# Kernel tuning notes

Hardware: AMD Instinct MI355X
Metric: run time of the kernel (lower is better)

## Reference

```python
import jax, jax.numpy as jnp
import numpy as np
from jax import lax


def _attend(Wq, bq, h, key_mat, value, mask):
    # key_mat: [B, A, T], value: [B, T, Vd], h: [B, H], mask: [B, T]
    q = h @ Wq.T + bq                             # [B, A]
    energy = jnp.einsum('ba,bat->bt', q, key_mat)  # [B, T]
    att = jax.nn.softmax(energy, axis=-1) * mask
    att = att / jnp.sum(att, axis=-1, keepdims=True)
    ctx = jnp.einsum('bt,btv->bv', att, value)     # [B, Vd]
    return att, ctx


def setup_inputs() -> dict:
    B, T, H, A, Vd, V, L = 32, 512, 512, 128, 512, 32000, 100
    CD = H + Vd  # concat_dim
    root = jax.random.key(0)
    ks = jax.random.split(root, 20)
    s = 0.02
    inp = {
        'key': jax.random.normal(ks[0], (B, A, T), jnp.float32),
        'value': jax.random.normal(ks[1], (B, T, Vd), jnp.float32),
        'Yinput': jax.random.randint(ks[2], (B, L), 0, V),
        'max_len': L,
        'src_lens': jax.random.randint(ks[3], (B,), 1, T + 1),
        'W_emb': jax.random.normal(ks[4], (V, H), jnp.float32) * s,
        'b_proj': jnp.zeros((V,), jnp.float32),
        'Wq': jax.random.normal(ks[5], (A, H), jnp.float32) * s,
        'bq': jnp.zeros((A,), jnp.float32),
        'W_ih': jax.random.normal(ks[6], (4 * H, CD), jnp.float32) * s,
        'W_hh': jax.random.normal(ks[7], (4 * H, H), jnp.float32) * s,
        'b_ih': jnp.zeros((4 * H,), jnp.float32),
        'b_hh': jnp.zeros((4 * H,), jnp.float32),
        'Wm': jax.random.normal(ks[8], (H, CD), jnp.float32) * s,
        'bm': jnp.zeros((H,), jnp.float32),
        'h00': jax.random.normal(ks[9], (1, H), jnp.float32) * s,
        'c00': jax.random.normal(ks[10], (1, H), jnp.float32) * s,
    }
    return inp


def reference(key, value, Yinput, max_len, src_lens, W_emb, b_proj, Wq, bq,
              W_ih, W_hh, b_ih, b_hh, Wm, bm, h00, c00):
    B, A, T = key.shape
    H = h00.shape[1]
    mask = (jnp.arange(T)[None, :] < src_lens[:, None]).astype(key.dtype)  # [B, T]

    h = jnp.broadcast_to(h00, (B, H))
    c = jnp.broadcast_to(c00, (B, H))
    _, ctx = _attend(Wq, bq, h, key, value, mask)
    idx = jnp.zeros((B,), jnp.int32)  # greedy decode, start token 0 (eval mode)

    def step(carry, _):
        h, c, ctx, idx = carry
        emb = W_emb[idx]                                   # [B, H]
        x = jnp.concatenate([emb, ctx], axis=-1)           # [B, H+Vd]
        # torch.nn.LSTMCell gate math (i, f, g, o order)
        gates = x @ W_ih.T + b_ih + h @ W_hh.T + b_hh      # [B, 4H]
        i, f, g, o = jnp.split(gates, 4, axis=-1)
        c1 = jax.nn.sigmoid(f) * c + jax.nn.sigmoid(i) * jnp.tanh(g)
        h1 = jax.nn.sigmoid(o) * jnp.tanh(c1)
        _, ctx1 = _attend(Wq, bq, h1, key, value, mask)
        cat2 = jnp.concatenate([c1, ctx1], axis=-1)        # note: uses c1 (as in source)
        proj = jax.nn.leaky_relu(cat2 @ Wm.T + bm, negative_slope=0.01)
        pred = jax.nn.log_softmax(proj @ W_emb.T + b_proj, axis=-1)  # tied weights
        idx1 = jnp.argmax(pred, axis=-1).astype(jnp.int32)
        return (h1, c1, ctx1, idx1), pred

    _, preds = lax.scan(step, (h, c, ctx, idx), None, length=int(max_len))
    return jnp.transpose(preds, (1, 0, 2))  # [B, max_len, V]
```

## Files before the change

### kernel.cpp

```cpp
#include <hip/hip_runtime.h>
#include <math.h>

#define B_  32
#define T_  512
#define H_  512
#define A_  128
#define VD_ 512
#define V_  32000
#define NCHUNK 500

__device__ __forceinline__ float sigf(float x){ return 1.f/(1.f+expf(-x)); }
__device__ __forceinline__ float dot4(float4 a, float4 b){ return a.x*b.x+a.y*b.y+a.z*b.z+a.w*b.w; }

struct DecArgs {
  const float *key, *value, *W_emb, *b_proj, *Wq, *bq, *W_ih, *W_hh, *b_ih, *b_hh, *Wm, *bm, *h00, *c00;
  const int* src_lens;
  float* out;
  float *hA, *hB, *c, *ctx, *projT, *logits, *lse, *pm, *ps;
  int *pidx, *idx;
  int L;
};

__global__ void k_init(DecArgs P) {
  int g = blockIdx.x*256 + threadIdx.x;
  if (g < B_*H_) { P.hA[g] = P.h00[g & (H_-1)]; P.c[g] = P.c00[g & (H_-1)]; }
  if (g < B_) P.idx[g] = 0;
}

__global__ __launch_bounds__(256) void k_gatesout(DecArgs P, const float* hin,
                                                  float* hout, int s) {
  __shared__ float sm[3200];
  int bid = blockIdx.x, tid = threadIdx.x;
  if (bid < 256) {
    float* Wl   = sm;
    float* xl   = sm + 576;
    float* part = sm + 2880;
    int*   idx_sh = (int*)(sm + 3168);
    const int kp = tid >> 5, jr = (tid >> 2) & 7, bg = tid & 3;
    if (tid < 32) idx_sh[tid] = P.idx[tid];
    float acc[8];
#pragma unroll
    for (int i = 0; i < 8; i++) acc[i] = 0.f;

    for (int w = 0; w < 24; w++) {
      __syncthreads();
      if (tid < 128) {
        int r = tid >> 4, i = tid & 15;
        int g = r >> 1, tl = r & 1;
        int j = g*512 + bid*2 + tl;
        const float4* src = (w < 16)
          ? (const float4*)(P.W_ih + (size_t)j*1024) + w*16 + i
          : (const float4*)(P.W_hh + (size_t)j*512) + (w-16)*16 + i;
        float4 x = *src;
        int kb = i*4;
        Wl[(kb+0)*9+r]=x.x; Wl[(kb+1)*9+r]=x.y; Wl[(kb+2)*9+r]=x.z; Wl[(kb+3)*9+r]=x.w;
      }
      {
        int q = tid*2;
#pragma unroll
        for (int u = 0; u < 2; u++, q++) {
          int b = q >> 4, i = q & 15;
          float4 x;
          if (w < 8)       x = *((const float4*)(P.W_emb + (size_t)idx_sh[b]*512) + w*16 + i);
          else if (w < 16) x = *((const float4*)(P.ctx + b*512) + (w-8)*16 + i);
          else             x = *((const float4*)(hin  + b*512) + (w-16)*16 + i);
          int kb = i*4;
          xl[(kb+0)*36+b]=x.x; xl[(kb+1)*36+b]=x.y; xl[(kb+2)*36+b]=x.z; xl[(kb+3)*36+b]=x.w;
        }
      }
      __syncthreads();
#pragma unroll
      for (int kk = 0; kk < 8; kk++) {
        int kl = kp*8 + kk;
        float wv = Wl[kl*9 + jr];
        const float4* xv = (const float4*)(xl + kl*36 + bg*8);
        float4 a0 = xv[0], a1 = xv[1];
        acc[0] += wv*a0.x; acc[1] += wv*a0.y; acc[2] += wv*a0.z; acc[3] += wv*a0.w;
        acc[4] += wv*a1.x; acc[5] += wv*a1.y; acc[6] += wv*a1.z; acc[7] += wv*a1.w;
      }
    }
    __syncthreads();
    for (int rd = 0; rd < 8; rd++) {
      if (kp == rd) {
        float* pr = part + jr*36 + bg*8;
        if (rd == 0) {
#pragma unroll
          for (int u = 0; u < 8; u++) pr[u] = acc[u];
        } else {
#pragma unroll
          for (int u = 0; u < 8; u++) pr[u] += acc[u];
        }
      }
      __syncthreads();
    }
    if (tid < 64) {
      int tl = tid >> 5, b = tid & 31;
      int t = bid*2 + tl;
      float gi = part[(0+tl)*36 + b] + P.b_ih[0*512+t] + P.b_hh[0*512+t];
      float gf = part[(2+tl)*36 + b] + P.b_ih[1*512+t] + P.b_hh[1*512+t];
      float gg = part[(4+tl)*36 + b] + P.b_ih[2*512+t] + P.b_hh[2*512+t];
      float go = part[(6+tl)*36 + b] + P.b_ih[3*512+t] + P.b_hh[3*512+t];
      float c0 = P.c[b*H_ + t];
      float c1 = sigf(gf)*c0 + sigf(gi)*tanhf(gg);
      P.c[b*H_ + t] = c1;
      hout[b*H_ + t] = sigf(go)*tanhf(c1);
    }
  } else if (s > 0) {
    int r = bid - 256;
    int bb = r >> 3, vs = r & 7;
    float l = P.lse[bb];
    const float4* lg = (const float4*)(P.logits + (size_t)bb*V_ + vs*4000);
    float4* o4 = (float4*)(P.out + ((size_t)bb*P.L + (s-1))*V_ + vs*4000);
    for (int i = tid; i < 1000; i += 256) {
      float4 x = lg[i];
      o4[i] = make_float4(x.x-l, x.y-l, x.z-l, x.w-l);
    }
  }
}

__global__ __launch_bounds__(256) void k_att(DecArgs P, const float* hsrc) {
  __shared__ float sf[1408];
  int bid = blockIdx.x, tid = threadIdx.x;
  int b = bid & 31, vs = bid >> 5;
  float* h_sh   = sf;
  float* q_sh   = sf + 512;
  float* red    = sf + 640;
  float* att_sh = sf + 896;
  h_sh[tid]       = hsrc[b*H_ + tid];
  h_sh[tid + 256] = hsrc[b*H_ + tid + 256];
  __syncthreads();
  if (tid < 128) {
    const float4* hv = (const float4*)h_sh;
    const float4* w  = (const float4*)(P.Wq + (size_t)tid*H_);
    float acc = P.bq[tid];
#pragma unroll 8
    for (int k = 0; k < 128; k++) acc += dot4(w[k], hv[k]);
    q_sh[tid] = acc;
  }
  __syncthreads();
  const float* kp = P.key + (size_t)b*A_*T_;
  float e0 = 0.f, e1 = 0.f;
#pragma unroll 8
  for (int a = 0; a < A_; a++) {
    float qa = q_sh[a];
    e0 += qa * kp[a*T_ + tid];
    e1 += qa * kp[a*T_ + tid + 256];
  }
  red[tid] = fmaxf(e0, e1);
  __syncthreads();
  for (int s2 = 128; s2 > 0; s2 >>= 1) { if (tid < s2) red[tid] = fmaxf(red[tid], red[tid+s2]); __syncthreads(); }
  float M = red[0];
  __syncthreads();
  int len = P.src_lens[b];
  float p0 = (tid       < len) ? expf(e0 - M) : 0.f;
  float p1 = (tid + 256 < len) ? expf(e1 - M) : 0.f;
  red[tid] = p0 + p1;
  __syncthreads();
  for (int s2 = 128; s2 > 0; s2 >>= 1) { if (tid < s2) red[tid] += red[tid+s2]; __syncthreads(); }
  float S = red[0];
  __syncthreads();
  att_sh[tid]       = p0 / S;
  att_sh[tid + 256] = p1 / S;
  __syncthreads();
  int vl = tid & 63, tq = tid >> 6;
  int v = vs*64 + vl;
  const float* vp = P.value + (size_t)b*T_*VD_ + v;
  float acc = 0.f;
  int t0 = tq*128;
#pragma unroll 8
  for (int t = t0; t < t0 + 128; t++) acc += att_sh[t] * vp[(size_t)t*VD_];
  red[tid] = acc;
  __syncthreads();
  if (tid < 64) P.ctx[b*VD_ + vs*64 + tid] = red[tid] + red[tid+64] + red[tid+128] + red[tid+192];
}

__global__ __launch_bounds__(256) void k_proj(DecArgs P) {
  __shared__ float sm[2600];
  int bid = blockIdx.x, tid = threadIdx.x;
  float* Wl   = sm;
  float* xl   = sm + 192;
  float* part = sm + 2496;
  const int kp = tid >> 5, ml = (tid >> 4) & 1, bg = tid & 15;
  float acc0 = 0.f, acc1 = 0.f;

  for (int w = 0; w < 16; w++) {
    __syncthreads();
    if (tid < 32) {
      int r = tid >> 4, i = tid & 15;
      float4 x = *((const float4*)(P.Wm + (size_t)(bid*2+r)*1024) + w*16 + i);
      int kb = i*4;
      Wl[(kb+0)*3+r]=x.x; Wl[(kb+1)*3+r]=x.y; Wl[(kb+2)*3+r]=x.z; Wl[(kb+3)*3+r]=x.w;
    }
    {
      int q = tid*2;
#pragma unroll
      for (int u = 0; u < 2; u++, q++) {
        int b = q >> 4, i = q & 15;
        float4 x = (w < 8) ? *((const float4*)(P.c + b*512) + w*16 + i)
                           : *((const float4*)(P.ctx + b*512) + (w-8)*16 + i);
        int kb = i*4;
        xl[(kb+0)*36+b]=x.x; xl[(kb+1)*36+b]=x.y; xl[(kb+2)*36+b]=x.z; xl[(kb+3)*36+b]=x.w;
      }
    }
    __syncthreads();
#pragma unroll
    for (int kk = 0; kk < 8; kk++) {
      int kl = kp*8 + kk;
      float wv = Wl[kl*3 + ml];
      acc0 += wv * xl[kl*36 + bg*2];
      acc1 += wv * xl[kl*36 + bg*2 + 1];
    }
  }
  __syncthreads();
  for (int rd = 0; rd < 8; rd++) {
    if (kp == rd) {
      float* pr = part + ml*36 + bg*2;
      if (rd == 0) { pr[0] = acc0; pr[1] = acc1; }
      else         { pr[0] += acc0; pr[1] += acc1; }
    }
    __syncthreads();
  }
  if (tid < 64) {
    int ml2 = tid >> 5, b = tid & 31;
    int m = bid*2 + ml2;
    float s = part[ml2*36 + b] + P.bm[m];
    P.projT[m*32 + b] = (s > 0.f) ? s : 0.01f*s;
  }
}

__global__ __launch_bounds__(256) void k_logits(DecArgs P) {
  __shared__ float sm[9600];
  int bid = blockIdx.x, tid = threadIdx.x;
  const int v0 = bid * 64;
  float* Wl   = sm;
  float* pl   = sm + 4352;
  float* part = sm + 6400;
  const int kp = tid >> 5, vg = (tid >> 2) & 7, bg = tid & 3;
  const int sr = tid >> 2, skq = tid & 3;
  float acc[64];
#pragma unroll
  for (int i = 0; i < 64; i++) acc[i] = 0.f;

  const float* wrow = P.W_emb + (size_t)(v0 + sr)*H_ + skq*16;
  const float4* pbase = (const float4*)P.projT;
  float4 t0 = *((const float4*)(wrow + 0));
  float4 t1 = *((const float4*)(wrow + 4));
  float4 t2 = *((const float4*)(wrow + 8));
  float4 t3 = *((const float4*)(wrow + 12));
  float4 u0 = pbase[tid];
  float4 u1 = pbase[tid + 256];

  for (int w = 0; w < 8; w++) {
    __syncthreads();
    int kb = skq*16;
    Wl[(kb+ 0)*68+sr]=t0.x; Wl[(kb+ 1)*68+sr]=t0.y; Wl[(kb+ 2)*68+sr]=t0.z; Wl[(kb+ 3)*68+sr]=t0.w;
    Wl[(kb+ 4)*68+sr]=t1.x; Wl[(kb+ 5)*68+sr]=t1.y; Wl[(kb+ 6)*68+sr]=t1.z; Wl[(kb+ 7)*68+sr]=t1.w;
    Wl[(kb+ 8)*68+sr]=t2.x; Wl[(kb+ 9)*68+sr]=t2.y; Wl[(kb+10)*68+sr]=t2.z; Wl[(kb+11)*68+sr]=t2.w;
    Wl[(kb+12)*68+sr]=t3.x; Wl[(kb+13)*68+sr]=t3.y; Wl[(kb+14)*68+sr]=t3.z; Wl[(kb+15)*68+sr]=t3.w;
    ((float4*)pl)[tid]       = u0;
    ((float4*)pl)[tid + 256] = u1;
    __syncthreads();
    if (w < 7) {
      const float* wn = wrow + (w+1)*64;
      t0 = *((const float4*)(wn + 0));
      t1 = *((const float4*)(wn + 4));
      t2 = *((const float4*)(wn + 8));
      t3 = *((const float4*)(wn + 12));
      u0 = pbase[(w+1)*512 + tid];
      u1 = pbase[(w+1)*512 + tid + 256];
    }
#pragma unroll
    for (int kk = 0; kk < 8; kk++) {
      int kl = kp*8 + kk;
      float4 wv0 = *((const float4*)(Wl + kl*68 + vg*8));
      float4 wv1 = *((const float4*)(Wl + kl*68 + vg*8 + 4));
      float4 pv0 = *((const float4*)(pl + kl*32 + bg*8));
      float4 pv1 = *((const float4*)(pl + kl*32 + bg*8 + 4));
      float wa[8] = {wv0.x,wv0.y,wv0.z,wv0.w,wv1.x,wv1.y,wv1.z,wv1.w};
      float pa[8] = {pv0.x,pv0.y,pv0.z,pv0.w,pv1.x,pv1.y,pv1.z,pv1.w};
#pragma unroll
      for (int i = 0; i < 8; i++)
#pragma unroll
        for (int j = 0; j < 8; j++)
          acc[i*8+j] += wa[i]*pa[j];
    }
  }
  __syncthreads();
  if (kp == 0) {
#pragma unroll
    for (int j = 0; j < 8; j++) {
      int b = bg*8 + j;
      *((float4*)(part + b*68 + vg*8))     = make_float4(acc[0*8+j], acc[1*8+j], acc[2*8+j], acc[3*8+j]);
      *((float4*)(part + b*68 + vg*8 + 4)) = make_float4(acc[4*8+j], acc[5*8+j], acc[6*8+j], acc[7*8+j]);
    }
  }
  __syncthreads();
  for (int rd = 1; rd < 8; rd++) {
    if (kp == rd) {
#pragma unroll
      for (int j = 0; j < 8; j++) {
        int b = bg*8 + j;
        float4* q0 = (float4*)(part + b*68 + vg*8);
        float4* q1 = q0 + 1;
        float4 a0 = *q0, a1 = *q1;
        a0.x += acc[0*8+j]; a0.y += acc[1*8+j]; a0.z += acc[2*8+j]; a0.w += acc[3*8+j];
        a1.x += acc[4*8+j]; a1.y += acc[5*8+j]; a1.z += acc[6*8+j]; a1.w += acc[7*8+j];
        *q0 = a0; *q1 = a1;
      }
    }
    __syncthreads();
  }
  int b = tid >> 3, vq = tid & 7;
  float4 pA = *((const float4*)(part + b*68 + vq*8));
  float4 pB = *((const float4*)(part + b*68 + vq*8 + 4));
  int vb = v0 + vq*8;
  float x[8] = {pA.x,pA.y,pA.z,pA.w,pB.x,pB.y,pB.z,pB.w};
#pragma unroll
  for (int i = 0; i < 8; i++) x[i] += P.b_proj[vb + i];
  *((float4*)(P.logits + (size_t)b*V_ + vb))     = make_float4(x[0],x[1],x[2],x[3]);
  *((float4*)(P.logits + (size_t)b*V_ + vb + 4)) = make_float4(x[4],x[5],x[6],x[7]);
  float m = x[0], s = 1.f; int mi = vb;
#pragma unroll
  for (int i = 1; i < 8; i++) {
    if (x[i] > m) { s = s*expf(m - x[i]) + 1.f; m = x[i]; mi = vb + i; }
    else          { s += expf(x[i] - m); }
  }
  float* rm = sm; float* rs = sm + 256; int* ri = (int*)(sm + 512);
  __syncthreads();
  rm[vq*32 + b] = m; rs[vq*32 + b] = s; ri[vq*32 + b] = mi;
  __syncthreads();
  if (tid < 32) {
    int bb = tid;
    float M = rm[bb], S = rs[bb]; int I = ri[bb];
#pragma unroll
    for (int g = 1; g < 8; g++) {
      float m2 = rm[g*32+bb], s2 = rs[g*32+bb]; int i2 = ri[g*32+bb];
      if (m2 > M)       { S = S*expf(M - m2) + s2; M = m2; I = i2; }
      else if (m2 == M) { S += s2; I = min(I, i2); }
      else              { S += s2*expf(m2 - M); }
    }
    P.pm[bid*32 + bb] = M; P.ps[bid*32 + bb] = S; P.pidx[bid*32 + bb] = I;
  }
}

__global__ __launch_bounds__(256) void k_merge(DecArgs P) {
  __shared__ float sfm[256], sfs[256];
  __shared__ int   sii[256];
  int b = blockIdx.x, tid = threadIdx.x;
  float M = P.pm[tid*32 + b], S = P.ps[tid*32 + b]; int I = P.pidx[tid*32 + b];
  int c2 = tid + 256;
  if (c2 < NCHUNK) {
    float m2 = P.pm[c2*32+b], s2 = P.ps[c2*32+b]; int i2 = P.pidx[c2*32+b];
    if (m2 > M)       { S = S*expf(M - m2) + s2; M = m2; I = i2; }
    else if (m2 == M) { S += s2; I = min(I, i2); }
    else              { S += s2*expf(m2 - M); }
  }
  sfm[tid] = M; sfs[tid] = S; sii[tid] = I;
  __syncthreads();
  for (int st = 128; st > 0; st >>= 1) {
    if (tid < st) {
      float m1 = sfm[tid], s1 = sfs[tid]; int i1 = sii[tid];
      float m2 = sfm[tid+st], s2 = sfs[tid+st]; int i2 = sii[tid+st];
      float Mn, Sn; int In;
      if (m2 > m1)      { Mn = m2; Sn = s1*expf(m1-m2) + s2; In = i2; }
      else if (m2 < m1) { Mn = m1; Sn = s1 + s2*expf(m2-m1); In = i1; }
      else              { Mn = m1; Sn = s1 + s2; In = min(i1, i2); }
      sfm[tid] = Mn; sfs[tid] = Sn; sii[tid] = In;
    }
    __syncthreads();
  }
  if (tid == 0) { P.lse[b] = sfm[0] + logf(sfs[0]); P.idx[b] = sii[0]; }
}

__global__ __launch_bounds__(256) void k_finalout(DecArgs P) {
  int bid = blockIdx.x, tid = threadIdx.x;
  int b = bid & 31, vs = bid >> 5;
  float l = P.lse[b];
  const float4* lg = (const float4*)(P.logits + (size_t)b*V_ + vs*4000);
  float4* o4 = (float4*)(P.out + ((size_t)b*P.L + (P.L-1))*V_ + vs*4000);
  for (int i = tid; i < 1000; i += 256) {
    float4 x = lg[i];
    o4[i] = make_float4(x.x-l, x.y-l, x.z-l, x.w-l);
  }
}

extern "C" void kernel_launch(void* const* d_in, const int* in_sizes, int n_in,
                              void* d_out, int out_size, void* d_ws, size_t ws_size,
                              hipStream_t stream) {
  DecArgs P;
  P.key      = (const float*)d_in[0];
  P.value    = (const float*)d_in[1];
  P.src_lens = (const int*)d_in[4];
  P.W_emb    = (const float*)d_in[5];
  P.b_proj   = (const float*)d_in[6];
  P.Wq       = (const float*)d_in[7];
  P.bq       = (const float*)d_in[8];
  P.W_ih     = (const float*)d_in[9];
  P.W_hh     = (const float*)d_in[10];
  P.b_ih     = (const float*)d_in[11];
  P.b_hh     = (const float*)d_in[12];
  P.Wm       = (const float*)d_in[13];
  P.bm       = (const float*)d_in[14];
  P.h00      = (const float*)d_in[15];
  P.c00      = (const float*)d_in[16];
  P.out      = (float*)d_out;
  P.L        = in_sizes[2] / B_;

  float* ws = (float*)d_ws;
  P.hA     = ws; ws += B_*H_;
  P.hB     = ws; ws += B_*H_;
  P.c      = ws; ws += B_*H_;
  P.ctx    = ws; ws += B_*VD_;
  P.projT  = ws; ws += H_*B_;
  P.lse    = ws; ws += 32;
  P.pm     = ws; ws += NCHUNK*B_;
  P.ps     = ws; ws += NCHUNK*B_;
  P.logits = ws; ws += (size_t)B_*V_;
  P.pidx   = (int*)ws; ws += NCHUNK*B_;
  P.idx    = (int*)ws;

  k_init<<<64, 256, 0, stream>>>(P);
  k_att<<<256, 256, 0, stream>>>(P, P.hA);

  for (int s = 0; s < P.L; s++) {
    const float* hin  = (s & 1) ? P.hB : P.hA;
    float*       hout = (s & 1) ? P.hA : P.hB;
    k_gatesout<<<512, 256, 0, stream>>>(P, hin, hout, s);
    k_att<<<256, 256, 0, stream>>>(P, hout);
    k_proj<<<256, 256, 0, stream>>>(P);
    k_logits<<<NCHUNK, 256, 0, stream>>>(P);
    k_merge<<<32, 256, 0, stream>>>(P);
  }
  k_finalout<<<256, 256, 0, stream>>>(P);
}
```

Measured before the change: 10.08 ms.

## Prefetch gate tiles into registers, widen attention grid, fold merge into logits

```diff
diff --git a/kernel.cpp b/kernel.cpp
--- a/kernel.cpp
+++ b/kernel.cpp
@@ -18,6 +18,7 @@
   float* out;
   float *hA, *hB, *c, *ctx, *projT, *logits, *lse, *pm, *ps;
   int *pidx, *idx;
+  int* bar;
   int L;
 };
 
@@ -41,34 +42,58 @@
     float acc[8];
 #pragma unroll
     for (int i = 0; i < 8; i++) acc[i] = 0.f;
+    __syncthreads();
+
+    const int r = tid >> 4, iW = tid & 15;
+    const int gW = r >> 1, tlW = r & 1;
+    const int jW = gW*512 + bid*2 + tlW;
+    float4 wreg; float4 xreg[2];
+    {
+      if (tid < 128) wreg = *((const float4*)(P.W_ih + (size_t)jW*1024) + iW);
+      int q = tid*2;
+#pragma unroll
+      for (int u = 0; u < 2; u++) {
+        int b = (q+u) >> 4, i = (q+u) & 15;
+        xreg[u] = *((const float4*)(P.W_emb + (size_t)idx_sh[b]*512) + i);
+      }
+    }
 
     for (int w = 0; w < 24; w++) {
       __syncthreads();
       if (tid < 128) {
-        int r = tid >> 4, i = tid & 15;
-        int g = r >> 1, tl = r & 1;
-        int j = g*512 + bid*2 + tl;
-        const float4* src = (w < 16)
-          ? (const float4*)(P.W_ih + (size_t)j*1024) + w*16 + i
-          : (const float4*)(P.W_hh + (size_t)j*512) + (w-16)*16 + i;
-        float4 x = *src;
-        int kb = i*4;
-        Wl[(kb+0)*9+r]=x.x; Wl[(kb+1)*9+r]=x.y; Wl[(kb+2)*9+r]=x.z; Wl[(kb+3)*9+r]=x.w;
+        int kb = iW*4;
+        Wl[(kb+0)*9+r]=wreg.x; Wl[(kb+1)*9+r]=wreg.y; Wl[(kb+2)*9+r]=wreg.z; Wl[(kb+3)*9+r]=wreg.w;
       }
       {
         int q = tid*2;
 #pragma unroll
-        for (int u = 0; u < 2; u++, q++) {
-          int b = q >> 4, i = q & 15;
-          float4 x;
-          if (w < 8)       x = *((const float4*)(P.W_emb + (size_t)idx_sh[b]*512) + w*16 + i);
-          else if (w < 16) x = *((const float4*)(P.ctx + b*512) + (w-8)*16 + i);
-          else             x = *((const float4*)(hin  + b*512) + (w-16)*16 + i);
+        for (int u = 0; u < 2; u++) {
+          int b = (q+u) >> 4, i = (q+u) & 15;
           int kb = i*4;
-          xl[(kb+0)*36+b]=x.x; xl[(kb+1)*36+b]=x.y; xl[(kb+2)*36+b]=x.z; xl[(kb+3)*36+b]=x.w;
+          xl[(kb+0)*36+b]=xreg[u].x; xl[(kb+1)*36+b]=xreg[u].y;
+          xl[(kb+2)*36+b]=xreg[u].z; xl[(kb+3)*36+b]=xreg[u].w;
         }
       }
       __syncthreads();
+      if (w < 23) {
+        int w1 = w + 1;
+        if (tid < 128) {
+          const float4* src = (w1 < 16)
+            ? (const float4*)(P.W_ih + (size_t)jW*1024) + w1*16 + iW
+            : (const float4*)(P.W_hh + (size_t)jW*512) + (w1-16)*16 + iW;
+          wreg = *src;
+        }
+        int q = tid*2;
+#pragma unroll
+        for (int u = 0; u < 2; u++) {
+          int b = (q+u) >> 4, i = (q+u) & 15;
+          const float4* src;
+          if (w1 < 8)       src = (const float4*)(P.W_emb + (size_t)idx_sh[b]*512) + w1*16 + i;
+          else if (w1 < 16) src = (const float4*)(P.ctx + b*512) + (w1-8)*16 + i;
+          else              src = (const float4*)(hin  + b*512) + (w1-16)*16 + i;
+          xreg[u] = *src;
+        }
+      }
 #pragma unroll
       for (int kk = 0; kk < 8; kk++) {
         int kl = kp*8 + kk;
@@ -106,8 +131,8 @@
       hout[b*H_ + t] = sigf(go)*tanhf(c1);
     }
   } else if (s > 0) {
-    int r = bid - 256;
-    int bb = r >> 3, vs = r & 7;
+    int r2 = bid - 256;
+    int bb = r2 >> 3, vs = r2 & 7;
     float l = P.lse[bb];
     const float4* lg = (const float4*)(P.logits + (size_t)bb*V_ + vs*4000);
     float4* o4 = (float4*)(P.out + ((size_t)bb*P.L + (s-1))*V_ + vs*4000);
@@ -129,14 +154,17 @@
   h_sh[tid]       = hsrc[b*H_ + tid];
   h_sh[tid + 256] = hsrc[b*H_ + tid + 256];
   __syncthreads();
-  if (tid < 128) {
-    const float4* hv = (const float4*)h_sh;
-    const float4* w  = (const float4*)(P.Wq + (size_t)tid*H_);
-    float acc = P.bq[tid];
+  {
+    int a = tid & 127, half = tid >> 7;
+    const float4* hv = (const float4*)h_sh + half*64;
+    const float4* w  = (const float4*)(P.Wq + (size_t)a*H_) + half*64;
+    float acc = 0.f;
 #pragma unroll 8
-    for (int k = 0; k < 128; k++) acc += dot4(w[k], hv[k]);
-    q_sh[tid] = acc;
-  }
+    for (int k = 0; k < 64; k++) acc += dot4(w[k], hv[k]);
+    red[tid] = acc;
+  }
+  __syncthreads();
+  if (tid < 128) q_sh[tid] = red[tid] + red[128 + tid] + P.bq[tid];
   __syncthreads();
   const float* kp = P.key + (size_t)b*A_*T_;
   float e0 = 0.f, e1 = 0.f;
@@ -146,6 +174,7 @@
     e0 += qa * kp[a*T_ + tid];
     e1 += qa * kp[a*T_ + tid + 256];
   }
+  __syncthreads();
   red[tid] = fmaxf(e0, e1);
   __syncthreads();
   for (int s2 = 128; s2 > 0; s2 >>= 1) { if (tid < s2) red[tid] = fmaxf(red[tid], red[tid+s2]); __syncthreads(); }
@@ -162,16 +191,20 @@
   att_sh[tid]       = p0 / S;
   att_sh[tid + 256] = p1 / S;
   __syncthreads();
-  int vl = tid & 63, tq = tid >> 6;
-  int v = vs*64 + vl;
-  const float* vp = P.value + (size_t)b*T_*VD_ + v;
+  int vl = tid & 31, tq = tid >> 5;
+  const float* vp = P.value + (size_t)b*T_*VD_ + vs*32 + vl;
   float acc = 0.f;
-  int t0 = tq*128;
+  int t0 = tq*64;
 #pragma unroll 8
-  for (int t = t0; t < t0 + 128; t++) acc += att_sh[t] * vp[(size_t)t*VD_];
+  for (int t = t0; t < t0 + 64; t++) acc += att_sh[t] * vp[(size_t)t*VD_];
   red[tid] = acc;
   __syncthreads();
-  if (tid < 64) P.ctx[b*VD_ + vs*64 + tid] = red[tid] + red[tid+64] + red[tid+128] + red[tid+192];
+  if (tid < 32) {
+    float s2 = 0.f;
+#pragma unroll
+    for (int j = 0; j < 8; j++) s2 += red[j*32 + tid];
+    P.ctx[b*VD_ + vs*32 + tid] = s2;
+  }
 }
 
 __global__ __launch_bounds__(256) void k_proj(DecArgs P) {
@@ -225,6 +258,30 @@
     int m = bid*2 + ml2;
     float s = part[ml2*36 + b] + P.bm[m];
     P.projT[m*32 + b] = (s > 0.f) ? s : 0.01f*s;
+  }
+}
+
+__device__ __forceinline__ void merge_all(const DecArgs& P, int tid, float* sm) {
+  int b = tid >> 3, g = tid & 7;
+  float M = -INFINITY, S = 0.f; int I = 0x7fffffff;
+  for (int ch = g; ch < NCHUNK; ch += 8) {
+    float m2 = P.pm[ch*32+b], s2 = P.ps[ch*32+b]; int i2 = P.pidx[ch*32+b];
+    if (m2 > M)       { S = S*expf(M-m2) + s2; M = m2; I = i2; }
+    else if (m2 == M) { S += s2; I = min(I, i2); }
+    else              { S += s2*expf(m2-M); }
+  }
+  float* mm = sm; float* ss = sm + 256; int* ii = (int*)(sm + 512);
+  mm[tid] = M; ss[tid] = S; ii[tid] = I;
+  __syncthreads();
+  if (g == 0) {
+    for (int j = 1; j < 8; j++) {
+      float m2 = mm[b*8+j], s2 = ss[b*8+j]; int i2 = ii[b*8+j];
+      if (m2 > M)       { S = S*expf(M-m2) + s2; M = m2; I = i2; }
+      else if (m2 == M) { S += s2; I = min(I, i2); }
+      else              { S += s2*expf(m2-M); }
+    }
+    P.lse[b] = M + logf(S);
+    P.idx[b] = I;
   }
 }
 
@@ -341,35 +398,19 @@
     }
     P.pm[bid*32 + bb] = M; P.ps[bid*32 + bb] = S; P.pidx[bid*32 + bb] = I;
   }
-}
-
-__global__ __launch_bounds__(256) void k_merge(DecArgs P) {
-  __shared__ float sfm[256], sfs[256];
-  __shared__ int   sii[256];
-  int b = blockIdx.x, tid = threadIdx.x;
-  float M = P.pm[tid*32 + b], S = P.ps[tid*32 + b]; int I = P.pidx[tid*32 + b];
-  int c2 = tid + 256;
-  if (c2 < NCHUNK) {
-    float m2 = P.pm[c2*32+b], s2 = P.ps[c2*32+b]; int i2 = P.pidx[c2*32+b];
-    if (m2 > M)       { S = S*expf(M - m2) + s2; M = m2; I = i2; }
-    else if (m2 == M) { S += s2; I = min(I, i2); }
-    else              { S += s2*expf(m2 - M); }
-  }
-  sfm[tid] = M; sfs[tid] = S; sii[tid] = I;
-  __syncthreads();
-  for (int st = 128; st > 0; st >>= 1) {
-    if (tid < st) {
-      float m1 = sfm[tid], s1 = sfs[tid]; int i1 = sii[tid];
-      float m2 = sfm[tid+st], s2 = sfs[tid+st]; int i2 = sii[tid+st];
-      float Mn, Sn; int In;
-      if (m2 > m1)      { Mn = m2; Sn = s1*expf(m1-m2) + s2; In = i2; }
-      else if (m2 < m1) { Mn = m1; Sn = s1 + s2*expf(m2-m1); In = i1; }
-      else              { Mn = m1; Sn = s1 + s2; In = min(i1, i2); }
-      sfm[tid] = Mn; sfs[tid] = Sn; sii[tid] = In;
-    }
-    __syncthreads();
-  }
-  if (tid == 0) { P.lse[b] = sfm[0] + logf(sfs[0]); P.idx[b] = sii[0]; }
+  __syncthreads();
+  if (tid == 0) {
+    int dc = __hip_atomic_fetch_add(P.bar, 1, __ATOMIC_ACQ_REL, __HIP_MEMORY_SCOPE_AGENT);
+    ((int*)(sm + 1024))[0] = (dc == NCHUNK - 1) ? 1 : 0;
+  }
+  __syncthreads();
+  int last = ((int*)(sm + 1024))[0];
+  __syncthreads();
+  if (last) {
+    merge_all(P, tid, sm);
+    __syncthreads();
+    if (tid == 0) __hip_atomic_store(P.bar, 0, __ATOMIC_RELAXED, __HIP_MEMORY_SCOPE_AGENT);
+  }
 }
 
 __global__ __launch_bounds__(256) void k_finalout(DecArgs P) {
@@ -406,7 +447,8 @@
   P.out      = (float*)d_out;
   P.L        = in_sizes[2] / B_;
 
-  float* ws = (float*)d_ws;
+  P.bar = (int*)d_ws;
+  float* ws = (float*)d_ws + 64;
   P.hA     = ws; ws += B_*H_;
   P.hB     = ws; ws += B_*H_;
   P.c      = ws; ws += B_*H_;
@@ -419,17 +461,17 @@
   P.pidx   = (int*)ws; ws += NCHUNK*B_;
   P.idx    = (int*)ws;
 
+  hipMemsetAsync(P.bar, 0, 64*sizeof(int), stream);
   k_init<<<64, 256, 0, stream>>>(P);
-  k_att<<<256, 256, 0, stream>>>(P, P.hA);
+  k_att<<<512, 256, 0, stream>>>(P, P.hA);
 
   for (int s = 0; s < P.L; s++) {
     const float* hin  = (s & 1) ? P.hB : P.hA;
     float*       hout = (s & 1) ? P.hA : P.hB;
     k_gatesout<<<512, 256, 0, stream>>>(P, hin, hout, s);
-    k_att<<<256, 256, 0, stream>>>(P, hout);
+    k_att<<<512, 256, 0, stream>>>(P, hout);
     k_proj<<<256, 256, 0, stream>>>(P);
     k_logits<<<NCHUNK, 256, 0, stream>>>(P);
-    k_merge<<<32, 256, 0, stream>>>(P);
   }
   k_finalout<<<256, 256, 0, stream>>>(P);
 }
```

Result: slower. 12.37 ms (+22.7%).
